# Kernel tuning notes

Hardware: AMD Instinct MI355X
Metric: run time of the kernel (lower is better)

## Reference

```python
import jax, jax.numpy as jnp
import numpy as np

N_NODES = 100000
N_EDGES = 1600000
IN_CH, HID_CH, OUT_CH = 128, 64, 64
NEG_SLOPE = 0.2
EPS = 1e-16


def setup_inputs() -> dict:
    key = jax.random.key(0)
    ks = jax.random.split(key, 10)
    x = jax.random.normal(ks[0], (N_NODES, IN_CH), dtype=jnp.float32)
    edge_index = jax.random.randint(ks[1], (2, N_EDGES), 0, N_NODES, dtype=jnp.int64)
    s1 = 1.0 / np.sqrt(IN_CH)
    s2 = 1.0 / np.sqrt(HID_CH)
    return {
        "x": x,
        "edge_index": edge_index,
        "W1": jax.random.normal(ks[2], (IN_CH, HID_CH), dtype=jnp.float32) * s1,
        "a_src1": jax.random.normal(ks[3], (HID_CH,), dtype=jnp.float32) * s2,
        "a_dst1": jax.random.normal(ks[4], (HID_CH,), dtype=jnp.float32) * s2,
        "b1": jnp.zeros((HID_CH,), dtype=jnp.float32),
        "W2": jax.random.normal(ks[5], (HID_CH, OUT_CH), dtype=jnp.float32) * s2,
        "a_src2": jax.random.normal(ks[6], (OUT_CH,), dtype=jnp.float32) * (1.0 / np.sqrt(OUT_CH)),
        "a_dst2": jax.random.normal(ks[7], (OUT_CH,), dtype=jnp.float32) * (1.0 / np.sqrt(OUT_CH)),
        "b2": jnp.zeros((OUT_CH,), dtype=jnp.float32),
    }


def gat_conv(x, src, dst, W, a_s, a_d, b):
    # node projection: [N, d_out]
    h = x @ W
    # per-node attention halves, gathered per edge
    alpha = jax.nn.leaky_relu((h @ a_s)[src] + (h @ a_d)[dst], NEG_SLOPE)  # [E]
    # segment softmax over edges grouped by destination node
    m = jax.ops.segment_max(alpha, dst, num_segments=N_NODES)
    e = jnp.exp(alpha - m[dst])
    z = jax.ops.segment_sum(e, dst, num_segments=N_NODES)
    w = e / (z[dst] + EPS)  # [E]
    # weighted scatter-sum of source features
    out = jax.ops.segment_sum(h[src] * w[:, None], dst, num_segments=N_NODES)
    return out + b


def reference(x, edge_index, W1, a_src1, a_dst1, b1, W2, a_src2, a_dst2, b2):
    # add self loops once (PyG add_self_loops=True in both convs)
    loops = jnp.arange(N_NODES, dtype=edge_index.dtype)
    src = jnp.concatenate([edge_index[0], loops])
    dst = jnp.concatenate([edge_index[1], loops])
    h = jax.nn.relu(gat_conv(x, src, dst, W1, a_src1, a_dst1, b1))
    return gat_conv(h, src, dst, W2, a_src2, a_dst2, b2)
```

## Files before the change

kernel.cpp:

```cpp
#include <hip/hip_runtime.h>
#include <cstdint>

#define NN 100000
#define NEG 0.2f

__global__ void k_detect(const void* e, int* mode) {
    if (threadIdx.x == 0 && blockIdx.x == 0) {
        const int* p = (const int*)e;
        int allz = 1;
        for (int i = 0; i < 64; ++i)
            if (p[2 * i + 1] != 0) { allz = 0; break; }
        mode[0] = allz;
    }
}

__device__ __forceinline__ void load_edge(const void* e, long E, long i, int is64,
                                          long& s, long& d) {
    if (is64) {
        const long long* p = (const long long*)e;
        s = (long)p[i]; d = (long)p[E + i];
    } else {
        const int* p = (const int*)e;
        s = p[i]; d = p[E + i];
    }
}

__global__ void k_init_cnt(int* cnt, int n) {
    int i = blockIdx.x * 256 + threadIdx.x;
    if (i < n) cnt[i] = 1;
}

__global__ void k_count(const void* e, long E, const int* mode, int* cnt, int n) {
    long i = (long)blockIdx.x * 256 + threadIdx.x;
    if (i >= E) return;
    int is64 = mode[0];
    long s, d;
    load_edge(e, E, i, is64, s, d);
    if ((unsigned long)s < (unsigned long)n && (unsigned long)d < (unsigned long)n)
        atomicAdd(&cnt[d], 1);
}

__global__ void k_scan_block(const int* cnt, int* excl, int* bsums, int n) {
    __shared__ int sm[256];
    int i = blockIdx.x * 256 + threadIdx.x;
    int v = (i < n) ? cnt[i] : 0;
    sm[threadIdx.x] = v;
    __syncthreads();
    for (int off = 1; off < 256; off <<= 1) {
        int t = (threadIdx.x >= off) ? sm[threadIdx.x - off] : 0;
        __syncthreads();
        sm[threadIdx.x] += t;
        __syncthreads();
    }
    if (i < n) excl[i] = sm[threadIdx.x] - v;
    if (threadIdx.x == 255) bsums[blockIdx.x] = sm[255];
}

__global__ void k_scan_bsums(int* bsums, int nb) {
    __shared__ int sm[512];
    int t = threadIdx.x;
    int v = (t < nb) ? bsums[t] : 0;
    sm[t] = v;
    __syncthreads();
    for (int off = 1; off < 512; off <<= 1) {
        int tv = (t >= off) ? sm[t - off] : 0;
        __syncthreads();
        sm[t] += tv;
        __syncthreads();
    }
    if (t < nb) bsums[t] = sm[t] - v;
}

__global__ void k_scan_add(int* rowptr, const int* bsums, const int* cnt, int n) {
    int i = blockIdx.x * 256 + threadIdx.x;
    if (i < n) {
        int v = rowptr[i] + bsums[blockIdx.x];
        rowptr[i] = v;
        if (i == n - 1) rowptr[n] = v + cnt[i];
    }
}

__global__ void k_fill_self(const int* rowptr, int* csr, int* cursor, int n) {
    int i = blockIdx.x * 256 + threadIdx.x;
    if (i < n) {
        csr[rowptr[i]] = i;
        cursor[i] = 1;
    }
}

__global__ void k_fill(const void* e, long E, const int* mode, const int* rowptr,
                       int* cursor, int* csr, int n) {
    long i = (long)blockIdx.x * 256 + threadIdx.x;
    if (i >= E) return;
    int is64 = mode[0];
    long s, d;
    load_edge(e, E, i, is64, s, d);
    if ((unsigned long)s < (unsigned long)n && (unsigned long)d < (unsigned long)n) {
        int slot = atomicAdd(&cursor[d], 1);
        csr[rowptr[d] + slot] = (int)s;
    }
}

template <int K>
__global__ __launch_bounds__(256) void k_gemm_attn(
    const float* __restrict__ X, const float* __restrict__ W,
    const float* __restrict__ As, const float* __restrict__ Ad,
    float* __restrict__ H, float* __restrict__ AS, float* __restrict__ AD, int n) {
    constexpr int KC = 32;
    __shared__ float Wl[KC * 64];
    __shared__ float Xt[KC][68];
    const int tid = threadIdx.x;
    const int tx = tid & 15, ty = tid >> 4;
    const long row0 = (long)blockIdx.x * 64;
    float acc[4][4] = {{0.f}};

    for (int k0 = 0; k0 < K; k0 += KC) {
        __syncthreads();
        {
            const float4* src = (const float4*)(W + (long)k0 * 64);
            float4* dst = (float4*)Wl;
            for (int i = tid; i < KC * 64 / 4; i += 256) dst[i] = src[i];
        }
        {
            const int rr = tid >> 3;
            const int kq = tid & 7;
#pragma unroll
            for (int h = 0; h < 2; ++h) {
                int r = rr + h * 32;
                long row = row0 + r;
                if (row >= n) row = n - 1;
                float4 v = *(const float4*)(X + row * K + k0 + kq * 4);
                Xt[kq * 4 + 0][r] = v.x;
                Xt[kq * 4 + 1][r] = v.y;
                Xt[kq * 4 + 2][r] = v.z;
                Xt[kq * 4 + 3][r] = v.w;
            }
        }
        __syncthreads();
#pragma unroll
        for (int kk = 0; kk < KC; ++kk) {
            float4 xv = *(const float4*)(&Xt[kk][ty * 4]);
            float4 wv = *(const float4*)(&Wl[kk * 64 + tx * 4]);
            acc[0][0] += xv.x * wv.x; acc[0][1] += xv.x * wv.y;
            acc[0][2] += xv.x * wv.z; acc[0][3] += xv.x * wv.w;
            acc[1][0] += xv.y * wv.x; acc[1][1] += xv.y * wv.y;
            acc[1][2] += xv.y * wv.z; acc[1][3] += xv.y * wv.w;
            acc[2][0] += xv.z * wv.x; acc[2][1] += xv.z * wv.y;
            acc[2][2] += xv.z * wv.z; acc[2][3] += xv.z * wv.w;
            acc[3][0] += xv.w * wv.x; acc[3][1] += xv.w * wv.y;
            acc[3][2] += xv.w * wv.z; acc[3][3] += xv.w * wv.w;
        }
    }

#pragma unroll
    for (int i = 0; i < 4; ++i) {
        long row = row0 + ty * 4 + i;
        if (row < n) {
            float4 o = {acc[i][0], acc[i][1], acc[i][2], acc[i][3]};
            *(float4*)(H + row * 64 + tx * 4) = o;
        }
    }
    float4 asv = *(const float4*)(As + tx * 4);
    float4 adv = *(const float4*)(Ad + tx * 4);
#pragma unroll
    for (int i = 0; i < 4; ++i) {
        float ps = acc[i][0] * asv.x + acc[i][1] * asv.y + acc[i][2] * asv.z + acc[i][3] * asv.w;
        float pd = acc[i][0] * adv.x + acc[i][1] * adv.y + acc[i][2] * adv.z + acc[i][3] * adv.w;
#pragma unroll
        for (int off = 1; off < 16; off <<= 1) {
            ps += __shfl_xor(ps, off);
            pd += __shfl_xor(pd, off);
        }
        if (tx == 0) {
            long row = row0 + ty * 4 + i;
            if (row < n) { AS[row] = ps; AD[row] = pd; }
        }
    }
}

__global__ __launch_bounds__(256) void k_agg(
    const int* __restrict__ rowptr, const int* __restrict__ csr,
    const float* __restrict__ AS, const float* __restrict__ AD,
    const float* __restrict__ H, const float* __restrict__ B,
    float* __restrict__ OUT, int n, int relu) {
    const int lane = threadIdx.x & 63;
    const int node = blockIdx.x * 4 + (threadIdx.x >> 6);
    if (node >= n) return;
    const int beg = rowptr[node], end = rowptr[node + 1];
    const int deg = end - beg;
    const float ad = AD[node];
    float acc = 0.f;

    if (deg <= 64) {
        const int idx = beg + lane;
        const bool v = idx < end;
        int s = v ? csr[idx] : 0;
        float a = v ? AS[s] + ad : -__builtin_inff();
        a = (a >= 0.f) ? a : NEG * a;
        float m = a;
#pragma unroll
        for (int off = 32; off; off >>= 1) m = fmaxf(m, __shfl_xor(m, off));
        float ez = v ? __expf(a - m) : 0.f;
        float z = ez;
#pragma unroll
        for (int off = 32; off; off >>= 1) z += __shfl_xor(z, off);
        float wgt = ez * (1.f / (z + 1e-16f));
        int j = 0;
        for (; j + 4 <= deg; j += 4) {
            int s0 = __shfl(s, j), s1 = __shfl(s, j + 1);
            int s2 = __shfl(s, j + 2), s3 = __shfl(s, j + 3);
            float w0 = __shfl(wgt, j), w1 = __shfl(wgt, j + 1);
            float w2 = __shfl(wgt, j + 2), w3 = __shfl(wgt, j + 3);
            float h0 = H[(long)s0 * 64 + lane];
            float h1 = H[(long)s1 * 64 + lane];
            float h2 = H[(long)s2 * 64 + lane];
            float h3 = H[(long)s3 * 64 + lane];
            acc += w0 * h0 + w1 * h1 + w2 * h2 + w3 * h3;
        }
        for (; j < deg; ++j) {
            int sj = __shfl(s, j);
            float wj = __shfl(wgt, j);
            acc += wj * H[(long)sj * 64 + lane];
        }
    } else {
        float m = -__builtin_inff(), z = 0.f;
        for (int p0 = beg; p0 < end; p0 += 64) {
            int idx = p0 + lane;
            float a = -__builtin_inff();
            if (idx < end) {
                int s = csr[idx];
                float t = AS[s] + ad;
                a = (t >= 0.f) ? t : NEG * t;
            }
            float cm = a;
#pragma unroll
            for (int off = 32; off; off >>= 1) cm = fmaxf(cm, __shfl_xor(cm, off));
            float mn = fmaxf(m, cm);
            float ez = (idx < end) ? __expf(a - mn) : 0.f;
#pragma unroll
            for (int off = 32; off; off >>= 1) ez += __shfl_xor(ez, off);
            z = (p0 == beg) ? ez : z * __expf(m - mn) + ez;
            m = mn;
        }
        const float invz = 1.f / (z + 1e-16f);
        for (int p0 = beg; p0 < end; p0 += 64) {
            int idx = p0 + lane;
            int s = 0; float wgt = 0.f;
            if (idx < end) {
                s = csr[idx];
                float a = AS[s] + ad;
                a = (a >= 0.f) ? a : NEG * a;
                wgt = __expf(a - m) * invz;
            }
            int cnt = min(64, end - p0);
            for (int j = 0; j < cnt; ++j) {
                int sj = __shfl(s, j);
                float wj = __shfl(wgt, j);
                acc += wj * H[(long)sj * 64 + lane];
            }
        }
    }
    acc += B[lane];
    if (relu) acc = fmaxf(acc, 0.f);
    OUT[(long)node * 64 + lane] = acc;
}

extern "C" void kernel_launch(void* const* d_in, const int* in_sizes, int n_in,
                              void* d_out, int out_size, void* d_ws, size_t ws_size,
                              hipStream_t stream) {
    const float* x   = (const float*)d_in[0];
    const void*  eix = d_in[1];
    const float* W1  = (const float*)d_in[2];
    const float* as1 = (const float*)d_in[3];
    const float* ad1 = (const float*)d_in[4];
    const float* b1  = (const float*)d_in[5];
    const float* W2  = (const float*)d_in[6];
    const float* as2 = (const float*)d_in[7];
    const float* ad2 = (const float*)d_in[8];
    const float* b2  = (const float*)d_in[9];
    float* out = (float*)d_out;

    const int  n = NN;
    const long E = (long)in_sizes[1] / 2;

    char* w = (char*)d_ws;
    size_t off = 0;
    auto alloc = [&](size_t bytes) -> void* {
        void* p = w + off;
        off = (off + bytes + 255) & ~(size_t)255;
        return p;
    };
    int*   mode   = (int*)alloc(4);
    int*   cnt    = (int*)alloc((size_t)n * 4);
    int*   rowptr = (int*)alloc((size_t)(n + 1) * 4);
    int*   cursor = (int*)alloc((size_t)n * 4);
    int*   bsums  = (int*)alloc(512 * 4);
    int*   csr    = (int*)alloc((size_t)(E + n) * 4);
    float* H      = (float*)alloc((size_t)n * 64 * 4);
    float* AS     = (float*)alloc((size_t)n * 4);
    float* AD     = (float*)alloc((size_t)n * 4);

    const int nbN = (n + 255) / 256;
    const int nbE = (int)((E + 255) / 256);
    const int nbG = (n + 63) / 64;

    k_detect<<<1, 64, 0, stream>>>(eix, mode);
    k_init_cnt<<<nbN, 256, 0, stream>>>(cnt, n);
    k_count<<<nbE, 256, 0, stream>>>(eix, E, mode, cnt, n);
    k_scan_block<<<nbN, 256, 0, stream>>>(cnt, rowptr, bsums, n);
    k_scan_bsums<<<1, 512, 0, stream>>>(bsums, nbN);
    k_scan_add<<<nbN, 256, 0, stream>>>(rowptr, bsums, cnt, n);
    k_fill_self<<<nbN, 256, 0, stream>>>(rowptr, csr, cursor, n);
    k_fill<<<nbE, 256, 0, stream>>>(eix, E, mode, rowptr, cursor, csr, n);

    k_gemm_attn<128><<<nbG, 256, 0, stream>>>(x, W1, as1, ad1, H, AS, AD, n);
    k_agg<<<(n + 3) / 4, 256, 0, stream>>>(rowptr, csr, AS, AD, H, b1, out, n, 1);
    k_gemm_attn<64><<<nbG, 256, 0, stream>>>(out, W2, as2, ad2, H, AS, AD, n);
    k_agg<<<(n + 3) / 4, 256, 0, stream>>>(rowptr, csr, AS, AD, H, b2, out, n, 0);
}
```

Baseline: 474.7 us.

## Shard CSR build counters across 8 copies to reduce atomic contention

```diff
diff --git a/kernel.cpp b/kernel.cpp
--- a/kernel.cpp
+++ b/kernel.cpp
@@ -2,6 +2,7 @@
 #include <cstdint>
 
 #define NN 100000
+#define NX 8
 #define NEG 0.2f
 
 __global__ void k_detect(const void* e, int* mode) {
@@ -14,33 +15,22 @@
     }
 }
 
-__device__ __forceinline__ void load_edge(const void* e, long E, long i, int is64,
-                                          long& s, long& d) {
-    if (is64) {
-        const long long* p = (const long long*)e;
-        s = (long)p[i]; d = (long)p[E + i];
-    } else {
-        const int* p = (const int*)e;
-        s = p[i]; d = p[E + i];
-    }
-}
-
-__global__ void k_init_cnt(int* cnt, int n) {
+__global__ void k_zero(int* p, int n) {
     int i = blockIdx.x * 256 + threadIdx.x;
-    if (i < n) cnt[i] = 1;
-}
-
-__global__ void k_count(const void* e, long E, const int* mode, int* cnt, int n) {
+    if (i < n) p[i] = 0;
+}
+
+__global__ void k_count(const void* e, long E, const int* mode, int* cnt) {
     long i = (long)blockIdx.x * 256 + threadIdx.x;
     if (i >= E) return;
-    int is64 = mode[0];
-    long s, d;
-    load_edge(e, E, i, is64, s, d);
-    if ((unsigned long)s < (unsigned long)n && (unsigned long)d < (unsigned long)n)
-        atomicAdd(&cnt[d], 1);
-}
-
-__global__ void k_scan_block(const int* cnt, int* excl, int* bsums, int n) {
+    const int x = (int)(blockIdx.x & (NX - 1));
+    long d;
+    if (mode[0]) d = (long)((const long long*)e)[E + i];
+    else         d = ((const int*)e)[E + i];
+    atomicAdd(&cnt[(long)x * NN + d], 1);
+}
+
+__global__ void k_scan_block(const int* cnt, int* S, int* bsums, int n) {
     __shared__ int sm[256];
     int i = blockIdx.x * 256 + threadIdx.x;
     int v = (i < n) ? cnt[i] : 0;
@@ -52,53 +42,54 @@
         sm[threadIdx.x] += t;
         __syncthreads();
     }
-    if (i < n) excl[i] = sm[threadIdx.x] - v;
+    if (i < n) S[i] = sm[threadIdx.x] - v;
     if (threadIdx.x == 255) bsums[blockIdx.x] = sm[255];
 }
 
-__global__ void k_scan_bsums(int* bsums, int nb) {
-    __shared__ int sm[512];
-    int t = threadIdx.x;
-    int v = (t < nb) ? bsums[t] : 0;
-    sm[t] = v;
+__global__ void k_scan_mid(int* bs, int nb) {
+    __shared__ int sm[1024];
+    __shared__ int carry_s;
+    const int t = threadIdx.x;
+    if (t == 0) carry_s = 0;
     __syncthreads();
-    for (int off = 1; off < 512; off <<= 1) {
-        int tv = (t >= off) ? sm[t - off] : 0;
-        __syncthreads();
-        sm[t] += tv;
-        __syncthreads();
-    }
-    if (t < nb) bsums[t] = sm[t] - v;
-}
-
-__global__ void k_scan_add(int* rowptr, const int* bsums, const int* cnt, int n) {
+    for (int r = 0; r * 1024 < nb; ++r) {
+        int i = r * 1024 + t;
+        int v = (i < nb) ? bs[i] : 0;
+        sm[t] = v;
+        __syncthreads();
+        for (int off = 1; off < 1024; off <<= 1) {
+            int tv = (t >= off) ? sm[t - off] : 0;
+            __syncthreads();
+            sm[t] += tv;
+            __syncthreads();
+        }
+        int carry = carry_s;
+        if (i < nb) bs[i] = sm[t] - v + carry;
+        __syncthreads();
+        if (t == 1023) carry_s = carry + sm[1023];
+        __syncthreads();
+    }
+}
+
+__global__ void k_scan_add(int* S, const int* bsums, int n) {
     int i = blockIdx.x * 256 + threadIdx.x;
-    if (i < n) {
-        int v = rowptr[i] + bsums[blockIdx.x];
-        rowptr[i] = v;
-        if (i == n - 1) rowptr[n] = v + cnt[i];
-    }
-}
-
-__global__ void k_fill_self(const int* rowptr, int* csr, int* cursor, int n) {
-    int i = blockIdx.x * 256 + threadIdx.x;
-    if (i < n) {
-        csr[rowptr[i]] = i;
-        cursor[i] = 1;
-    }
-}
-
-__global__ void k_fill(const void* e, long E, const int* mode, const int* rowptr,
-                       int* cursor, int* csr, int n) {
+    if (i < n) S[i] += bsums[blockIdx.x];
+}
+
+__global__ void k_fill(const void* e, long E, const int* mode, int* S, int* csr) {
     long i = (long)blockIdx.x * 256 + threadIdx.x;
     if (i >= E) return;
-    int is64 = mode[0];
+    const int x = (int)(blockIdx.x & (NX - 1));
     long s, d;
-    load_edge(e, E, i, is64, s, d);
-    if ((unsigned long)s < (unsigned long)n && (unsigned long)d < (unsigned long)n) {
-        int slot = atomicAdd(&cursor[d], 1);
-        csr[rowptr[d] + slot] = (int)s;
-    }
+    if (mode[0]) {
+        const long long* p = (const long long*)e;
+        s = (long)p[i]; d = (long)p[E + i];
+    } else {
+        const int* p = (const int*)e;
+        s = p[i]; d = p[E + i];
+    }
+    int pos = atomicAdd(&S[(long)x * NN + d], 1);
+    csr[pos] = (int)s;
 }
 
 template <int K>
@@ -179,22 +170,45 @@
 }
 
 __global__ __launch_bounds__(256) void k_agg(
-    const int* __restrict__ rowptr, const int* __restrict__ csr,
+    const int* __restrict__ cnt, const int* __restrict__ S,
+    const int* __restrict__ csr,
     const float* __restrict__ AS, const float* __restrict__ AD,
     const float* __restrict__ H, const float* __restrict__ B,
     float* __restrict__ OUT, int n, int relu) {
     const int lane = threadIdx.x & 63;
     const int node = blockIdx.x * 4 + (threadIdx.x >> 6);
     if (node >= n) return;
-    const int beg = rowptr[node], end = rowptr[node + 1];
-    const int deg = end - beg;
+
+    int cx[NX], sx[NX];
+#pragma unroll
+    for (int x = 0; x < NX; ++x) {
+        int c = cnt[x * NN + node];
+        int en = S[x * NN + node];
+        cx[x] = c;
+        sx[x] = en - c;
+    }
+    int degI = 0;
+#pragma unroll
+    for (int x = 0; x < NX; ++x) degI += cx[x];
+    const int degT = degI + 1;
     const float ad = AD[node];
+
+    auto lookup = [&](int e) -> int {
+        if (e >= degI) return node;
+        int addr = 0, cum = 0;
+#pragma unroll
+        for (int x = 0; x < NX; ++x) {
+            int o = e - cum;
+            if (o >= 0 && o < cx[x]) addr = sx[x] + o;
+            cum += cx[x];
+        }
+        return csr[addr];
+    };
+
     float acc = 0.f;
-
-    if (deg <= 64) {
-        const int idx = beg + lane;
-        const bool v = idx < end;
-        int s = v ? csr[idx] : 0;
+    if (degT <= 64) {
+        const bool v = lane < degT;
+        int s = lookup(lane);
         float a = v ? AS[s] + ad : -__builtin_inff();
         a = (a >= 0.f) ? a : NEG * a;
         float m = a;
@@ -206,7 +220,7 @@
         for (int off = 32; off; off >>= 1) z += __shfl_xor(z, off);
         float wgt = ez * (1.f / (z + 1e-16f));
         int j = 0;
-        for (; j + 4 <= deg; j += 4) {
+        for (; j + 4 <= degT; j += 4) {
             int s0 = __shfl(s, j), s1 = __shfl(s, j + 1);
             int s2 = __shfl(s, j + 2), s3 = __shfl(s, j + 3);
             float w0 = __shfl(wgt, j), w1 = __shfl(wgt, j + 1);
@@ -217,43 +231,42 @@
             float h3 = H[(long)s3 * 64 + lane];
             acc += w0 * h0 + w1 * h1 + w2 * h2 + w3 * h3;
         }
-        for (; j < deg; ++j) {
+        for (; j < degT; ++j) {
             int sj = __shfl(s, j);
             float wj = __shfl(wgt, j);
             acc += wj * H[(long)sj * 64 + lane];
         }
     } else {
         float m = -__builtin_inff(), z = 0.f;
-        for (int p0 = beg; p0 < end; p0 += 64) {
-            int idx = p0 + lane;
-            float a = -__builtin_inff();
-            if (idx < end) {
-                int s = csr[idx];
-                float t = AS[s] + ad;
-                a = (t >= 0.f) ? t : NEG * t;
-            }
+        for (int p0 = 0; p0 < degT; p0 += 64) {
+            int e = p0 + lane;
+            bool v = e < degT;
+            int s = lookup(e);
+            float a = v ? AS[s] + ad : -__builtin_inff();
+            a = (a >= 0.f) ? a : NEG * a;
             float cm = a;
 #pragma unroll
             for (int off = 32; off; off >>= 1) cm = fmaxf(cm, __shfl_xor(cm, off));
             float mn = fmaxf(m, cm);
-            float ez = (idx < end) ? __expf(a - mn) : 0.f;
+            float ez = v ? __expf(a - mn) : 0.f;
 #pragma unroll
             for (int off = 32; off; off >>= 1) ez += __shfl_xor(ez, off);
-            z = (p0 == beg) ? ez : z * __expf(m - mn) + ez;
+            z = (p0 == 0) ? ez : z * __expf(m - mn) + ez;
             m = mn;
         }
         const float invz = 1.f / (z + 1e-16f);
-        for (int p0 = beg; p0 < end; p0 += 64) {
-            int idx = p0 + lane;
-            int s = 0; float wgt = 0.f;
-            if (idx < end) {
-                s = csr[idx];
+        for (int p0 = 0; p0 < degT; p0 += 64) {
+            int e = p0 + lane;
+            bool v = e < degT;
+            int s = lookup(e);
+            float wgt = 0.f;
+            if (v) {
                 float a = AS[s] + ad;
                 a = (a >= 0.f) ? a : NEG * a;
                 wgt = __expf(a - m) * invz;
             }
-            int cnt = min(64, end - p0);
-            for (int j = 0; j < cnt; ++j) {
+            int cntv = min(64, degT - p0);
+            for (int j = 0; j < cntv; ++j) {
                 int sj = __shfl(s, j);
                 float wj = __shfl(wgt, j);
                 acc += wj * H[(long)sj * 64 + lane];
@@ -280,8 +293,9 @@
     const float* b2  = (const float*)d_in[9];
     float* out = (float*)d_out;
 
-    const int  n = NN;
-    const long E = (long)in_sizes[1] / 2;
+    const int  n  = NN;
+    const long E  = (long)in_sizes[1] / 2;
+    const int  NS = NX * NN;
 
     char* w = (char*)d_ws;
     size_t off = 0;
@@ -290,31 +304,29 @@
         off = (off + bytes + 255) & ~(size_t)255;
         return p;
     };
-    int*   mode   = (int*)alloc(4);
-    int*   cnt    = (int*)alloc((size_t)n * 4);
-    int*   rowptr = (int*)alloc((size_t)(n + 1) * 4);
-    int*   cursor = (int*)alloc((size_t)n * 4);
-    int*   bsums  = (int*)alloc(512 * 4);
-    int*   csr    = (int*)alloc((size_t)(E + n) * 4);
-    float* H      = (float*)alloc((size_t)n * 64 * 4);
-    float* AS     = (float*)alloc((size_t)n * 4);
-    float* AD     = (float*)alloc((size_t)n * 4);
-
-    const int nbN = (n + 255) / 256;
+    int*   mode  = (int*)alloc(4);
+    int*   cnt   = (int*)alloc((size_t)NS * 4);
+    int*   S     = (int*)alloc((size_t)NS * 4);
+    int*   bsums = (int*)alloc(4096 * 4);
+    int*   csr   = (int*)alloc((size_t)E * 4);
+    float* H     = (float*)alloc((size_t)n * 64 * 4);
+    float* AS    = (float*)alloc((size_t)n * 4);
+    float* AD    = (float*)alloc((size_t)n * 4);
+
+    const int nbS = (NS + 255) / 256;
     const int nbE = (int)((E + 255) / 256);
     const int nbG = (n + 63) / 64;
 
     k_detect<<<1, 64, 0, stream>>>(eix, mode);
-    k_init_cnt<<<nbN, 256, 0, stream>>>(cnt, n);
-    k_count<<<nbE, 256, 0, stream>>>(eix, E, mode, cnt, n);
-    k_scan_block<<<nbN, 256, 0, stream>>>(cnt, rowptr, bsums, n);
-    k_scan_bsums<<<1, 512, 0, stream>>>(bsums, nbN);
-    k_scan_add<<<nbN, 256, 0, stream>>>(rowptr, bsums, cnt, n);
-    k_fill_self<<<nbN, 256, 0, stream>>>(rowptr, csr, cursor, n);
-    k_fill<<<nbE, 256, 0, stream>>>(eix, E, mode, rowptr, cursor, csr, n);
+    k_zero<<<nbS, 256, 0, stream>>>(cnt, NS);
+    k_count<<<nbE, 256, 0, stream>>>(eix, E, mode, cnt);
+    k_scan_block<<<nbS, 256, 0, stream>>>(cnt, S, bsums, NS);
+    k_scan_mid<<<1, 1024, 0, stream>>>(bsums, nbS);
+    k_scan_add<<<nbS, 256, 0, stream>>>(S, bsums, NS);
+    k_fill<<<nbE, 256, 0, stream>>>(eix, E, mode, S, csr);
 
     k_gemm_attn<128><<<nbG, 256, 0, stream>>>(x, W1, as1, ad1, H, AS, AD, n);
-    k_agg<<<(n + 3) / 4, 256, 0, stream>>>(rowptr, csr, AS, AD, H, b1, out, n, 1);
+    k_agg<<<(n + 3) / 4, 256, 0, stream>>>(cnt, S, csr, AS, AD, H, b1, out, n, 1);
     k_gemm_attn<64><<<nbG, 256, 0, stream>>>(out, W2, as2, ad2, H, AS, AD, n);
-    k_agg<<<(n + 3) / 4, 256, 0, stream>>>(rowptr, csr, AS, AD, H, b2, out, n, 0);
-}
+    k_agg<<<(n + 3) / 4, 256, 0, stream>>>(cnt, S, csr, AS, AD, H, b2, out, n, 0);
+}
```

Result: faster. 463.1 us (-2.4%).
